# Performance work log

Hardware: AMD Instinct MI355X
Metric: run time of the kernel (lower is better)

The kernel has to match this reference:

```python
import jax, jax.numpy as jnp
import numpy as np

B, T, D = 32, 2048, 512
U = 512              # units per direction (output_dim // 2)
LEAKY = 0.9
CONNECTIVITY = 0.1
SPECTRAL_RADIUS = 0.95


def _make_recurrent(rng, units):
    # dense draw, sparsify by connectivity mask, rescale to target spectral radius
    w = rng.uniform(-1.0, 1.0, size=(units, units)).astype(np.float32)
    mask = (rng.uniform(size=(units, units)) < CONNECTIVITY).astype(np.float32)
    w = w * mask
    eig = np.max(np.abs(np.linalg.eigvals(w)))
    w = w * (SPECTRAL_RADIUS / max(eig, 1e-8))
    return w.astype(np.float32)


def setup_inputs() -> dict:
    key = jax.random.key(0)
    kx, kf, kb = jax.random.split(key, 3)
    rng = np.random.default_rng(0)
    limit = np.sqrt(6.0 / (D + U)).astype(np.float32)  # Glorot uniform
    x = jax.random.normal(kx, (B, T, D), dtype=jnp.float32)
    kernel_f = jax.random.uniform(kf, (D, U), minval=-limit, maxval=limit, dtype=jnp.float32)
    kernel_b = jax.random.uniform(kb, (D, U), minval=-limit, maxval=limit, dtype=jnp.float32)
    rec_f = jnp.asarray(_make_recurrent(rng, U))
    rec_b = jnp.asarray(_make_recurrent(rng, U))
    bias_f = jnp.zeros((U,), dtype=jnp.float32)
    bias_b = jnp.zeros((U,), dtype=jnp.float32)
    return {"x": x, "kernel_f": kernel_f, "rec_f": rec_f, "bias_f": bias_f,
            "kernel_b": kernel_b, "rec_b": rec_b, "bias_b": bias_b}


def _esn_scan(x, kernel, rec, bias):
    # x: [B, T, D] -> states [B, T, U]
    # precompute input projection for all steps (one big GEMM)
    xin = jnp.einsum('btd,du->btu', x, kernel) + bias  # [B, T, U]

    def step(h, u_t):
        h_new = (1.0 - LEAKY) * h + LEAKY * jnp.tanh(u_t + h @ rec)
        return h_new, h_new

    h0 = jnp.zeros((x.shape[0], rec.shape[0]), dtype=x.dtype)
    _, ys = jax.lax.scan(step, h0, jnp.swapaxes(xin, 0, 1))  # ys: [T, B, U]
    return jnp.swapaxes(ys, 0, 1)


def reference(x, kernel_f, rec_f, bias_f, kernel_b, rec_b, bias_b):
    out_f = _esn_scan(x, kernel_f, rec_f, bias_f)                       # [B, T, U]
    # backward layer: process time-reversed sequence, then reverse output back
    out_b = _esn_scan(x[:, ::-1, :], kernel_b, rec_b, bias_b)[:, ::-1, :]
    return jnp.concatenate([out_f, out_b], axis=-1)                     # [B, T, 2U]
```

## Files before the change

kernel.cpp:

```cpp
#include <hip/hip_runtime.h>

#define MAXNZ 96
#define NPAIR 48

typedef unsigned short u16;
typedef unsigned int u32;

__global__ __launch_bounds__(512) void esn_prep(
    const float* __restrict__ rec_f, const float* __restrict__ rec_b,
    float* __restrict__ wsv, u16* __restrict__ wsi, int* __restrict__ wscnt)
{
    const int dir = blockIdx.x;
    const int u = threadIdx.x;
    const float* rec = dir ? rec_b : rec_f;
    int cnt = 0;
    for (int k = 0; k < 512; ++k) {
        float v = rec[k * 512 + u];
        if (v != 0.0f && cnt < MAXNZ) {
            wsv[(dir * MAXNZ + cnt) * 512 + u] = v;
            wsi[(dir * MAXNZ + cnt) * 512 + u] = (u16)k;
            ++cnt;
        }
    }
    wscnt[dir * 512 + u] = cnt;
    for (int i = cnt; i < MAXNZ; ++i) {
        wsv[(dir * MAXNZ + i) * 512 + u] = 0.0f;
        wsi[(dir * MAXNZ + i) * 512 + u] = 0;
    }
}

__global__ __launch_bounds__(256) void esn_proj(
    const float* __restrict__ x,
    const float* __restrict__ kf, const float* __restrict__ kb,
    const float* __restrict__ bf, const float* __restrict__ bb,
    float* __restrict__ out)
{
    __shared__ float As[16][132];
    __shared__ float Bs[16][132];
    const int tid = threadIdx.x;
    const int bm = blockIdx.x;
    const int bn = blockIdx.y;
    const float* B    = (bn < 4) ? kf : kb;
    const float* bias = (bn < 4) ? bf : bb;
    const int colBase = (bn & 3) * 128;

    const int tm = tid >> 4;
    const int tn = tid & 15;

    float acc[8][8];
#pragma unroll
    for (int i = 0; i < 8; ++i)
#pragma unroll
        for (int j = 0; j < 8; ++j) acc[i][j] = 0.0f;

    const long aRow0 = (long)bm * 128;

    for (int k0 = 0; k0 < 512; k0 += 16) {
#pragma unroll
        for (int s = 0; s < 2; ++s) {
            int slot = tid + s * 256;
            int row = slot >> 2, c4 = slot & 3;
            float4 v = *(const float4*)&x[(aRow0 + row) * 512 + k0 + c4 * 4];
            As[c4 * 4 + 0][row] = v.x;
            As[c4 * 4 + 1][row] = v.y;
            As[c4 * 4 + 2][row] = v.z;
            As[c4 * 4 + 3][row] = v.w;
        }
#pragma unroll
        for (int s = 0; s < 2; ++s) {
            int slot = tid + s * 256;
            int kk = slot >> 5, c4 = slot & 31;
            *(float4*)&Bs[kk][c4 * 4] =
                *(const float4*)&B[(long)(k0 + kk) * 512 + colBase + c4 * 4];
        }
        __syncthreads();
#pragma unroll
        for (int k = 0; k < 16; ++k) {
            float a[8], b[8];
            *(float4*)&a[0] = *(const float4*)&As[k][tm * 4];
            *(float4*)&a[4] = *(const float4*)&As[k][64 + tm * 4];
            *(float4*)&b[0] = *(const float4*)&Bs[k][tn * 4];
            *(float4*)&b[4] = *(const float4*)&Bs[k][64 + tn * 4];
#pragma unroll
            for (int i = 0; i < 8; ++i)
#pragma unroll
                for (int j = 0; j < 8; ++j)
                    acc[i][j] += a[i] * b[j];
        }
        __syncthreads();
    }

#pragma unroll
    for (int jj = 0; jj < 2; ++jj) {
        float bv[4];
#pragma unroll
        for (int j = 0; j < 4; ++j) bv[j] = bias[colBase + jj * 64 + tn * 4 + j];
#pragma unroll
        for (int ii = 0; ii < 2; ++ii) {
#pragma unroll
            for (int i = 0; i < 4; ++i) {
                long r = aRow0 + ii * 64 + tm * 4 + i;
                float4 v;
                v.x = acc[ii * 4 + i][jj * 4 + 0] + bv[0];
                v.y = acc[ii * 4 + i][jj * 4 + 1] + bv[1];
                v.z = acc[ii * 4 + i][jj * 4 + 2] + bv[2];
                v.w = acc[ii * 4 + i][jj * 4 + 3] + bv[3];
                *(float4*)&out[r * 1024 + bn * 128 + jj * 64 + tn * 4] = v;
            }
        }
    }
}

__global__ __launch_bounds__(512) void esn_scan(
    const float* __restrict__ wsv, const u16* __restrict__ wsi,
    const int* __restrict__ wscnt, float* __restrict__ io)
{
    const int sid = blockIdx.x;
    const int dir = sid & 1;
    const int b = sid >> 1;
    const int u = threadIdx.x;

    __shared__ float h[2][512];

    float vals[MAXNZ];
    u32 poff[NPAIR];
    {
        const float* vb = wsv + (long)dir * MAXNZ * 512 + u;
        const u16* ib = wsi + (long)dir * MAXNZ * 512 + u;
#pragma unroll
        for (int i = 0; i < MAXNZ; ++i) vals[i] = vb[i * 512];
#pragma unroll
        for (int i = 0; i < NPAIR; ++i) {
            u32 o0 = ib[(2 * i) * 512];
            u32 o1 = ib[(2 * i + 1) * 512];
            poff[i] = o0 | (o1 << 16);
        }
    }
    int cmax = wscnt[dir * 512 + u];
#pragma unroll
    for (int d = 1; d < 64; d <<= 1) {
        int o = __shfl_xor(cmax, d, 64);
        cmax = cmax > o ? cmax : o;
    }

    h[0][u] = 0.0f;
    float hreg = 0.0f;
    __syncthreads();

    const long rowStep = dir ? -1024L : 1024L;
    long rowCur = ((long)b * 2048 + (dir ? 2047 : 0)) * 1024 + dir * 512 + u;
    float ucur = io[rowCur];
    long rowNext = rowCur + rowStep;

    for (int t = 0; t < 2048; ++t) {
        float unext = 0.0f;
        if (t < 2047) unext = io[rowNext];

        const float* hc = h[t & 1];
        float acc0 = ucur, acc1 = 0.0f;
#pragma unroll
        for (int blk = 0; blk < 6; ++blk) {
            if (blk * 16 < cmax) {
#pragma unroll
                for (int q = 0; q < 8; ++q) {
                    const int i = blk * 8 + q;
                    u32 p = poff[i];
                    acc0 += vals[2 * i]     * hc[p & 0xffffu];
                    acc1 += vals[2 * i + 1] * hc[p >> 16];
                }
            }
        }
        float acc = acc0 + acc1;
        float e = __builtin_exp2f(acc * 2.8853900817779268f);
        float r = __builtin_amdgcn_rcpf(e + 1.0f);
        float th = 1.0f - 2.0f * r;
        float hn = 0.1f * hreg + 0.9f * th;

        io[rowCur] = hn;
        h[(t + 1) & 1][u] = hn;
        hreg = hn;
        __syncthreads();

        ucur = unext;
        rowCur = rowNext;
        rowNext += rowStep;
    }
}

extern "C" void kernel_launch(void* const* d_in, const int* in_sizes, int n_in,
                              void* d_out, int out_size, void* d_ws, size_t ws_size,
                              hipStream_t stream) {
    const float* x  = (const float*)d_in[0];
    const float* kf = (const float*)d_in[1];
    const float* rf = (const float*)d_in[2];
    const float* bf = (const float*)d_in[3];
    const float* kb = (const float*)d_in[4];
    const float* rb = (const float*)d_in[5];
    const float* bb = (const float*)d_in[6];
    float* out = (float*)d_out;

    float* wsv = (float*)d_ws;
    u16*   wsi = (u16*)((char*)d_ws + 2 * MAXNZ * 512 * 4);
    int* wscnt = (int*)((char*)d_ws + 2 * MAXNZ * 512 * 6);

    esn_prep<<<2, 512, 0, stream>>>(rf, rb, wsv, wsi, wscnt);
    esn_proj<<<dim3(512, 8), 256, 0, stream>>>(x, kf, kb, bf, bb, out);
    esn_scan<<<64, 512, 0, stream>>>(wsv, wsi, wscnt, out);
}
```

Before: 4.496 ms.

## Assign sparse slots per wavefront to balance LDS banks in scan gathers

Result: slower. 6.909 ms (+53.7%).

```diff
diff --git a/kernel.cpp b/kernel.cpp
--- a/kernel.cpp
+++ b/kernel.cpp
@@ -5,28 +5,53 @@
 
 typedef unsigned short u16;
 typedef unsigned int u32;
-
-__global__ __launch_bounds__(512) void esn_prep(
+typedef unsigned long long u64;
+
+__global__ __launch_bounds__(64) void esn_prep(
     const float* __restrict__ rec_f, const float* __restrict__ rec_b,
     float* __restrict__ wsv, u16* __restrict__ wsi, int* __restrict__ wscnt)
 {
-    const int dir = blockIdx.x;
-    const int u = threadIdx.x;
+    const int dir  = blockIdx.x >> 3;
+    const int wg   = blockIdx.x & 7;
+    const int lane = threadIdx.x;
+    const int col  = wg * 64 + lane;
     const float* rec = dir ? rec_b : rec_f;
-    int cnt = 0;
+
+    __shared__ u32 cnt[MAXNZ][32];
+    for (int i = lane; i < MAXNZ * 32; i += 64) ((u32*)cnt)[i] = 0;
+    __syncthreads();
+
+    for (int s = 0; s < MAXNZ; ++s) {
+        wsv[(dir * MAXNZ + s) * 512 + col] = 0.0f;
+        wsi[(dir * MAXNZ + s) * 512 + col] = (u16)(col & 31);
+    }
+
+    u64 used0 = 0, used1 = 0;
+    int maxslot = -1;
     for (int k = 0; k < 512; ++k) {
-        float v = rec[k * 512 + u];
-        if (v != 0.0f && cnt < MAXNZ) {
-            wsv[(dir * MAXNZ + cnt) * 512 + u] = v;
-            wsi[(dir * MAXNZ + cnt) * 512 + u] = (u16)k;
-            ++cnt;
-        }
-    }
-    wscnt[dir * 512 + u] = cnt;
-    for (int i = cnt; i < MAXNZ; ++i) {
-        wsv[(dir * MAXNZ + i) * 512 + u] = 0.0f;
-        wsi[(dir * MAXNZ + i) * 512 + u] = 0;
-    }
+        float v = rec[k * 512 + col];
+        if (v == 0.0f) continue;
+        const int bank = k & 31;
+        int s = -1;
+#pragma unroll 1
+        for (int capi = 0; capi < 3 && s < 0; ++capi) {
+            const u32 cap = (capi == 0) ? 2u : ((capi == 1) ? 4u : 64u);
+#pragma unroll 1
+            for (int t = 0; t < MAXNZ; ++t) {
+                bool used = (t < 64) ? ((used0 >> t) & 1) : ((used1 >> (t - 64)) & 1);
+                if (used) continue;
+                u32 old = atomicAdd(&cnt[t][bank], 1);
+                if (old < cap) { s = t; break; }
+                atomicSub(&cnt[t][bank], 1);
+            }
+        }
+        if (s < 0) continue;
+        if (s < 64) used0 |= (1ull << s); else used1 |= (1ull << (s - 64));
+        if (s > maxslot) maxslot = s;
+        wsv[(dir * MAXNZ + s) * 512 + col] = v;
+        wsi[(dir * MAXNZ + s) * 512 + col] = (u16)k;
+    }
+    wscnt[dir * 512 + col] = maxslot + 1;
 }
 
 __global__ __launch_bounds__(256) void esn_proj(
@@ -203,7 +228,7 @@
     u16*   wsi = (u16*)((char*)d_ws + 2 * MAXNZ * 512 * 4);
     int* wscnt = (int*)((char*)d_ws + 2 * MAXNZ * 512 * 6);
 
-    esn_prep<<<2, 512, 0, stream>>>(rf, rb, wsv, wsi, wscnt);
+    esn_prep<<<16, 64, 0, stream>>>(rf, rb, wsv, wsi, wscnt);
     esn_proj<<<dim3(512, 8), 256, 0, stream>>>(x, kf, kb, bf, bb, out);
     esn_scan<<<64, 512, 0, stream>>>(wsv, wsi, wscnt, out);
 }
```
